# Kernel optimization log

Measured on AMD Instinct MI355X. Metric: run time of the kernel, lower is better.

Reference implementation:

```python
import jax, jax.numpy as jnp
import numpy as np

THRESH = 0.5  # original code thresholds raw span logit channel 0 at 0.5


def setup_inputs() -> dict:
    key = jax.random.key(0)
    ks = jax.random.split(key, 9)
    B, S, H, P = 4, 256, 768, 54  # P = num_spo_patterns + 1
    scale = 0.02
    return {
        "sequence_output": jax.random.normal(ks[0], (B, S, H), jnp.float32),
        "W1s": jax.random.normal(ks[1], (H, H), jnp.float32) * scale,
        "b1s": jnp.zeros((H,), jnp.float32),
        "W2s": jax.random.normal(ks[2], (2, H), jnp.float32) * scale,
        "b2s": jnp.zeros((2,), jnp.float32),
        "Wp1": jax.random.normal(ks[3], (H, 2 * H), jnp.float32) * scale,
        "bp1": jnp.zeros((H,), jnp.float32),
        "Wp2": jax.random.normal(ks[4], (P, H), jnp.float32) * scale,
        "bp2": jnp.zeros((P,), jnp.float32),
    }


def reference(sequence_output, W1s, b1s, W2s, b2s, Wp1, bp1, Wp2, bp2):
    x = sequence_output                                # [B,S,H]
    B, S, H = x.shape
    # span classifier: Linear -> ReLU -> Linear
    h = jax.nn.relu(jnp.einsum('bsh,kh->bsk', x, W1s) + b1s)
    span_logits = jnp.einsum('bsh,kh->bsk', h, W2s) + b2s   # [B,S,2]
    cand = span_logits[..., 0] > THRESH                      # [B,S] candidates
    # spo pattern classifier on concat pairs: Linear(2H,H) splits into two H->H maps
    Wa, Wb = Wp1[:, :H], Wp1[:, H:]                          # subject / object halves
    ha = jnp.einsum('bsh,kh->bsk', x, Wa)                    # [B,S,H]
    hb = jnp.einsum('bsh,kh->bsk', x, Wb)                    # [B,S,H]
    pair_hidden = jax.nn.relu(ha[:, :, None, :] + hb[:, None, :, :] + bp1)  # [B,S,S,H]
    pair_logits = jnp.einsum('bijh,ph->bijp', pair_hidden, Wp2) + bp2       # [B,S,S,P]
    # valid pairs: both are candidates and subj != obj (diagonal excluded)
    not_diag = ~jnp.eye(S, dtype=bool)
    valid = cand[:, :, None] & cand[:, None, :] & not_diag   # [B,S,S]
    # dense masked equivalent of the per-pair Python loop (invalid pairs zeroed,
    # matching the zeros fallback for empty candidate sets)
    spo_pattern_logits = jnp.where(valid[..., None], pair_logits, 0.0)
    return spo_pattern_logits
```

## Files before the change

kernel.cpp:

```cpp
#include <hip/hip_runtime.h>
#include <hip/hip_bf16.h>


#define M_ROWS 1024
#define HDIM 768
#define PDIM 54
#define MAXC 256
#define KSPLIT 4
#define KSEG (HDIM / KSPLIT)

#define CANDCNT_OFF  0
#define CANDIDX_OFF  1024
#define CANDSLOT_OFF 8192
#define HA_OFF       16384
#define HB_OFF       (16384 + 786432)
#define HPART_OFF    (16384 + 2 * 786432)

__global__ __launch_bounds__(256) void gemm_k_kernel(
    const float* __restrict__ x, const float* __restrict__ W1,
    float* __restrict__ hpart, int* __restrict__ candCnt)
{
    __shared__ float As[16][68];
    __shared__ float Bs[16][68];

    if (threadIdx.x == 0 && blockIdx.x == 0 && blockIdx.y == 0 && blockIdx.z == 0)
        *candCnt = 0;

    const int m0 = blockIdx.x * 64;
    const int n0 = blockIdx.y * 64;
    const int kb = blockIdx.z * KSEG;
    const int t  = threadIdx.x;
    const int tm = t & 15;
    const int tn = t >> 4;
    const int r  = t >> 2;
    const int c4 = (t & 3) * 4;

    float acc[4][4] = {};

    for (int k0 = kb; k0 < kb + KSEG; k0 += 16) {
        float4 av = *(const float4*)(x  + (size_t)(m0 + r) * HDIM + k0 + c4);
        float4 bv = *(const float4*)(W1 + (size_t)(n0 + r) * HDIM + k0 + c4);
        As[c4+0][r] = av.x; As[c4+1][r] = av.y; As[c4+2][r] = av.z; As[c4+3][r] = av.w;
        Bs[c4+0][r] = bv.x; Bs[c4+1][r] = bv.y; Bs[c4+2][r] = bv.z; Bs[c4+3][r] = bv.w;
        __syncthreads();
        #pragma unroll
        for (int kk = 0; kk < 16; ++kk) {
            float a[4], b[4];
            *(float4*)a = *(const float4*)&As[kk][tm * 4];
            *(float4*)b = *(const float4*)&Bs[kk][tn * 4];
            #pragma unroll
            for (int i = 0; i < 4; ++i)
                #pragma unroll
                for (int j = 0; j < 4; ++j)
                    acc[i][j] += a[i] * b[j];
        }
        __syncthreads();
    }

    float* dst = hpart + (size_t)blockIdx.z * (M_ROWS * HDIM);
    #pragma unroll
    for (int i = 0; i < 4; ++i) {
        float4 v = make_float4(acc[i][0], acc[i][1], acc[i][2], acc[i][3]);
        *(float4*)(dst + (size_t)(m0 + tm * 4 + i) * HDIM + n0 + tn * 4) = v;
    }
}

__global__ __launch_bounds__(256) void span_cand_kernel(
    const float* __restrict__ hpart, const float* __restrict__ b1,
    const float* __restrict__ w2row, const float* __restrict__ b2,
    int* __restrict__ candCount, int* __restrict__ candIdx,
    int* __restrict__ candSlot)
{
    const int m = blockIdx.x;
    const int t = threadIdx.x;
    float p = 0.f;
    for (int n = t; n < HDIM; n += 256) {
        float v = hpart[(size_t)m * HDIM + n]
                + hpart[(size_t)(M_ROWS * HDIM) + (size_t)m * HDIM + n]
                + hpart[(size_t)(2 * M_ROWS * HDIM) + (size_t)m * HDIM + n]
                + hpart[(size_t)(3 * M_ROWS * HDIM) + (size_t)m * HDIM + n];
        v += b1[n];
        v = v > 0.f ? v : 0.f;
        p += v * w2row[n];
    }
    __shared__ float wred[4];
    #pragma unroll
    for (int off = 32; off > 0; off >>= 1) p += __shfl_down(p, off, 64);
    if ((t & 63) == 0) wred[t >> 6] = p;
    __syncthreads();
    if (t == 0) {
        float s = wred[0] + wred[1] + wred[2] + wred[3] + b2[0];
        if (s > 0.5f) {
            int sl = atomicAdd(candCount, 1);
            if (sl < MAXC) { candIdx[sl] = m; candSlot[m] = sl; }
            else candSlot[m] = -1;
        } else {
            candSlot[m] = -1;
        }
    }
}

__global__ __launch_bounds__(256) void hab_kernel(
    const float* __restrict__ x, const float* __restrict__ Wp1,
    const int* __restrict__ candCount, const int* __restrict__ candIdx,
    float* __restrict__ ha, float* __restrict__ hb)
{
    int nc = *candCount; if (nc > MAXC) nc = MAXC;
    const int kk   = threadIdx.x >> 5;
    const int lane = threadIdx.x & 31;
    const int k    = blockIdx.x * 8 + kk;

    const float* wr = Wp1 + (size_t)k * (2 * HDIM);
    float4 wa[6], wb[6];
    #pragma unroll
    for (int c = 0; c < 6; ++c) {
        wa[c] = *(const float4*)(wr + c * 128 + lane * 4);
        wb[c] = *(const float4*)(wr + HDIM + c * 128 + lane * 4);
    }

    for (int slot = 0; slot < nc; ++slot) {
        int row = candIdx[slot];
        const float* xr = x + (size_t)row * HDIM;
        float sa = 0.f, sb = 0.f;
        #pragma unroll
        for (int c = 0; c < 6; ++c) {
            float4 xv = *(const float4*)(xr + c * 128 + lane * 4);
            sa += wa[c].x*xv.x + wa[c].y*xv.y + wa[c].z*xv.z + wa[c].w*xv.w;
            sb += wb[c].x*xv.x + wb[c].y*xv.y + wb[c].z*xv.z + wb[c].w*xv.w;
        }
        #pragma unroll
        for (int off = 16; off > 0; off >>= 1) {
            sa += __shfl_down(sa, off, 32);
            sb += __shfl_down(sb, off, 32);
        }
        if (lane == 0) {
            ha[(size_t)slot * HDIM + k] = sa;
            hb[(size_t)slot * HDIM + k] = sb;
        }
    }
}

__global__ __launch_bounds__(256) void pair_kernel(
    const float* __restrict__ ha, const float* __restrict__ hb,
    const float* __restrict__ bp1, const float* __restrict__ Wp2,
    const float* __restrict__ bp2, const int* __restrict__ candSlot,
    float* __restrict__ out)
{
    __shared__ int plist[512];
    __shared__ int pcnt;
    __shared__ float v[HDIM];
    __shared__ float red[4][PDIM + 2];
    const int t = threadIdx.x;

    float* outb = out + (size_t)blockIdx.x * 512 * PDIM;
    float4 z = make_float4(0.f, 0.f, 0.f, 0.f);
    #pragma unroll
    for (int q = 0; q < 27; ++q)
        *(float4*)(outb + (size_t)(q * 256 + t) * 4) = z;

    if (t == 0) pcnt = 0;
    __syncthreads();

    #pragma unroll
    for (int q = 0; q < 2; ++q) {
        int idx = blockIdx.x * 512 + q * 256 + t;
        int b = idx >> 16;
        int i = (idx >> 8) & 255;
        int j = idx & 255;
        if (i != j && candSlot[b * 256 + i] >= 0 && candSlot[b * 256 + j] >= 0) {
            int p = atomicAdd(&pcnt, 1);
            plist[p] = idx;
        }
    }
    __syncthreads();
    const int np = pcnt;

    for (int p = 0; p < np; ++p) {
        int idx = plist[p];
        int b = idx >> 16;
        int i = (idx >> 8) & 255;
        int j = idx & 255;
        int si = candSlot[b * 256 + i];
        int sj = candSlot[b * 256 + j];
        if (t < 192) {
            float4 a4 = *(const float4*)(ha + (size_t)si * HDIM + t * 4);
            float4 b4 = *(const float4*)(hb + (size_t)sj * HDIM + t * 4);
            float4 c4 = *(const float4*)(bp1 + t * 4);
            float4 r;
            r.x = a4.x + b4.x + c4.x; r.x = r.x > 0.f ? r.x : 0.f;
            r.y = a4.y + b4.y + c4.y; r.y = r.y > 0.f ? r.y : 0.f;
            r.z = a4.z + b4.z + c4.z; r.z = r.z > 0.f ? r.z : 0.f;
            r.w = a4.w + b4.w + c4.w; r.w = r.w > 0.f ? r.w : 0.f;
            *(float4*)(v + t * 4) = r;
        }
        __syncthreads();
        if (t < 216) {
            int pp  = t % PDIM;
            int seg = t / PDIM;
            const float* w  = Wp2 + (size_t)pp * HDIM + seg * 192;
            const float* vv = v + seg * 192;
            float s = 0.f;
            for (int h = 0; h < 192; h += 4) {
                float4 a  = *(const float4*)(vv + h);
                float4 b2 = *(const float4*)(w + h);
                s += a.x * b2.x + a.y * b2.y + a.z * b2.z + a.w * b2.w;
            }
            red[seg][pp] = s;
        }
        __syncthreads();
        if (t < PDIM)
            out[(size_t)idx * PDIM + t] = red[0][t] + red[1][t] + red[2][t] + red[3][t] + bp2[t];
        __syncthreads();
    }
}

extern "C" void kernel_launch(void* const* d_in, const int* in_sizes, int n_in,
                              void* d_out, int out_size, void* d_ws, size_t ws_size,
                              hipStream_t stream) {
    const float* x   = (const float*)d_in[0];
    const float* W1s = (const float*)d_in[1];
    const float* b1s = (const float*)d_in[2];
    const float* W2s = (const float*)d_in[3];
    const float* b2s = (const float*)d_in[4];
    const float* Wp1 = (const float*)d_in[5];
    const float* bp1 = (const float*)d_in[6];
    const float* Wp2 = (const float*)d_in[7];
    const float* bp2 = (const float*)d_in[8];

    char* ws = (char*)d_ws;
    int*   candCnt  = (int*)(ws + CANDCNT_OFF);
    int*   candIdx  = (int*)(ws + CANDIDX_OFF);
    int*   candSlot = (int*)(ws + CANDSLOT_OFF);
    float* ha       = (float*)(ws + HA_OFF);
    float* hb       = (float*)(ws + HB_OFF);
    float* hpart    = (float*)(ws + HPART_OFF);
    float* out = (float*)d_out;

    dim3 g(M_ROWS / 64, HDIM / 64, KSPLIT);
    gemm_k_kernel<<<g, 256, 0, stream>>>(x, W1s, hpart, candCnt);

    span_cand_kernel<<<M_ROWS, 256, 0, stream>>>(hpart, b1s, W2s, b2s,
                                                 candCnt, candIdx, candSlot);

    hab_kernel<<<96, 256, 0, stream>>>(x, Wp1, candCnt, candIdx, ha, hb);

    pair_kernel<<<512, 256, 0, stream>>>(ha, hb, bp1, Wp2, bp2, candSlot, out);
}
```

Baseline: 147.4 us.

## Fuse four stages into one cooperative persistent kernel with grid syncs

Replaces the four separate launches (split-K GEMM, span candidate scoring, ha/hb projection, pair classifier) with a single cooperative kernel of 768 blocks that uses grid.sync between phases. It also spreads the ha/hb projection over 8x more blocks by striding candidate slots, and halves the pair chunk size to 256 pairs per block. The goal is to remove launch gaps and the underutilised 96-block hab stage. In exchange it adds grid-wide barriers and requires all 768 blocks to be co-resident, falling back to the old launches if the cooperative launch fails.

```diff
diff --git a/kernel.cpp b/kernel.cpp
--- a/kernel.cpp
+++ b/kernel.cpp
@@ -1,5 +1,7 @@
 #include <hip/hip_runtime.h>
 #include <hip/hip_bf16.h>
+#include <hip/hip_cooperative_groups.h>
+namespace cg = cooperative_groups;
 
 
 #define M_ROWS 1024
@@ -8,6 +10,7 @@
 #define MAXC 256
 #define KSPLIT 4
 #define KSEG (HDIM / KSPLIT)
+#define GRID_C 768
 
 #define CANDCNT_OFF  0
 #define CANDIDX_OFF  1024
@@ -16,27 +19,213 @@
 #define HB_OFF       (16384 + 786432)
 #define HPART_OFF    (16384 + 2 * 786432)
 
+union SMem {
+    struct { float As[16][68]; float Bs[16][68]; } g;
+    struct { float wred[4]; } s;
+    struct { float v[HDIM]; float red[4][PDIM + 2]; int plist[256]; int pcnt; } p;
+};
+
+__global__ __launch_bounds__(256) void fused_kernel(
+    const float* __restrict__ x, const float* __restrict__ W1,
+    const float* __restrict__ b1, const float* __restrict__ w2row,
+    const float* __restrict__ b2, const float* __restrict__ Wp1,
+    const float* __restrict__ bp1, const float* __restrict__ Wp2,
+    const float* __restrict__ bp2,
+    float* __restrict__ hpart, int* __restrict__ candCnt,
+    int* __restrict__ candIdx, int* __restrict__ candSlot,
+    float* __restrict__ ha, float* __restrict__ hb,
+    float* __restrict__ out)
+{
+    __shared__ SMem sm;
+    cg::grid_group grid = cg::this_grid();
+    const int bid = blockIdx.x;
+    const int t   = threadIdx.x;
+
+    if (bid == 0 && t == 0) *candCnt = 0;
+    {
+        const int mt = bid & 15;
+        const int nt = (bid >> 4) % 12;
+        const int z  = bid / 192;
+        const int m0 = mt * 64, n0 = nt * 64, kb = z * KSEG;
+        const int tm = t & 15, tn = t >> 4;
+        const int r  = t >> 2, c4 = (t & 3) * 4;
+
+        float acc[4][4] = {};
+        for (int k0 = kb; k0 < kb + KSEG; k0 += 16) {
+            float4 av = *(const float4*)(x  + (size_t)(m0 + r) * HDIM + k0 + c4);
+            float4 bv = *(const float4*)(W1 + (size_t)(n0 + r) * HDIM + k0 + c4);
+            sm.g.As[c4+0][r] = av.x; sm.g.As[c4+1][r] = av.y; sm.g.As[c4+2][r] = av.z; sm.g.As[c4+3][r] = av.w;
+            sm.g.Bs[c4+0][r] = bv.x; sm.g.Bs[c4+1][r] = bv.y; sm.g.Bs[c4+2][r] = bv.z; sm.g.Bs[c4+3][r] = bv.w;
+            __syncthreads();
+            #pragma unroll
+            for (int kk = 0; kk < 16; ++kk) {
+                float a[4], b[4];
+                *(float4*)a = *(const float4*)&sm.g.As[kk][tm * 4];
+                *(float4*)b = *(const float4*)&sm.g.Bs[kk][tn * 4];
+                #pragma unroll
+                for (int i = 0; i < 4; ++i)
+                    #pragma unroll
+                    for (int j = 0; j < 4; ++j)
+                        acc[i][j] += a[i] * b[j];
+            }
+            __syncthreads();
+        }
+        float* dst = hpart + (size_t)z * (M_ROWS * HDIM);
+        #pragma unroll
+        for (int i = 0; i < 4; ++i) {
+            float4 v = make_float4(acc[i][0], acc[i][1], acc[i][2], acc[i][3]);
+            *(float4*)(dst + (size_t)(m0 + tm * 4 + i) * HDIM + n0 + tn * 4) = v;
+        }
+    }
+    grid.sync();
+
+    for (int m = bid; m < M_ROWS; m += GRID_C) {
+        float p = 0.f;
+        for (int n = t; n < HDIM; n += 256) {
+            float v = hpart[(size_t)m * HDIM + n]
+                    + hpart[(size_t)(M_ROWS * HDIM) + (size_t)m * HDIM + n]
+                    + hpart[(size_t)(2 * M_ROWS * HDIM) + (size_t)m * HDIM + n]
+                    + hpart[(size_t)(3 * M_ROWS * HDIM) + (size_t)m * HDIM + n];
+            v += b1[n];
+            v = v > 0.f ? v : 0.f;
+            p += v * w2row[n];
+        }
+        #pragma unroll
+        for (int off = 32; off > 0; off >>= 1) p += __shfl_down(p, off, 64);
+        if ((t & 63) == 0) sm.s.wred[t >> 6] = p;
+        __syncthreads();
+        if (t == 0) {
+            float s = sm.s.wred[0] + sm.s.wred[1] + sm.s.wred[2] + sm.s.wred[3] + b2[0];
+            if (s > 0.5f) {
+                int sl = atomicAdd(candCnt, 1);
+                if (sl < MAXC) { candIdx[sl] = m; candSlot[m] = sl; }
+                else candSlot[m] = -1;
+            } else {
+                candSlot[m] = -1;
+            }
+        }
+        __syncthreads();
+    }
+    grid.sync();
+
+    {
+        int nc = *candCnt; if (nc > MAXC) nc = MAXC;
+        const int kc   = bid % 96;
+        const int s0   = bid / 96;
+        const int kk   = t >> 5;
+        const int lane = t & 31;
+        const int k    = kc * 8 + kk;
+
+        const float* wr = Wp1 + (size_t)k * (2 * HDIM);
+        float4 wa[6], wb[6];
+        #pragma unroll
+        for (int c = 0; c < 6; ++c) {
+            wa[c] = *(const float4*)(wr + c * 128 + lane * 4);
+            wb[c] = *(const float4*)(wr + HDIM + c * 128 + lane * 4);
+        }
+        for (int slot = s0; slot < nc; slot += 8) {
+            int row = candIdx[slot];
+            const float* xr = x + (size_t)row * HDIM;
+            float sa = 0.f, sb = 0.f;
+            #pragma unroll
+            for (int c = 0; c < 6; ++c) {
+                float4 xv = *(const float4*)(xr + c * 128 + lane * 4);
+                sa += wa[c].x*xv.x + wa[c].y*xv.y + wa[c].z*xv.z + wa[c].w*xv.w;
+                sb += wb[c].x*xv.x + wb[c].y*xv.y + wb[c].z*xv.z + wb[c].w*xv.w;
+            }
+            #pragma unroll
+            for (int off = 16; off > 0; off >>= 1) {
+                sa += __shfl_down(sa, off, 32);
+                sb += __shfl_down(sb, off, 32);
+            }
+            if (lane == 0) {
+                ha[(size_t)slot * HDIM + k] = sa;
+                hb[(size_t)slot * HDIM + k] = sb;
+            }
+        }
+    }
+    grid.sync();
+
+    for (int chunk = bid; chunk < 1024; chunk += GRID_C) {
+        float* outb = out + (size_t)chunk * 256 * PDIM;
+        float4 z4 = make_float4(0.f, 0.f, 0.f, 0.f);
+        #pragma unroll
+        for (int q = 0; q < 14; ++q) {
+            int idx4 = q * 256 + t;
+            if (idx4 < 3456) *(float4*)(outb + (size_t)idx4 * 4) = z4;
+        }
+        if (t == 0) sm.p.pcnt = 0;
+        __syncthreads();
+
+        {
+            int idx = chunk * 256 + t;
+            int b = idx >> 16;
+            int i = (idx >> 8) & 255;
+            int j = idx & 255;
+            if (i != j && candSlot[b * 256 + i] >= 0 && candSlot[b * 256 + j] >= 0) {
+                int p = atomicAdd(&sm.p.pcnt, 1);
+                sm.p.plist[p] = idx;
+            }
+        }
+        __syncthreads();
+        const int np = sm.p.pcnt;
+
+        for (int p = 0; p < np; ++p) {
+            int idx = sm.p.plist[p];
+            int b = idx >> 16;
+            int i = (idx >> 8) & 255;
+            int j = idx & 255;
+            int si = candSlot[b * 256 + i];
+            int sj = candSlot[b * 256 + j];
+            if (t < 192) {
+                float4 a4 = *(const float4*)(ha + (size_t)si * HDIM + t * 4);
+                float4 b4 = *(const float4*)(hb + (size_t)sj * HDIM + t * 4);
+                float4 c4 = *(const float4*)(bp1 + t * 4);
+                float4 r;
+                r.x = a4.x + b4.x + c4.x; r.x = r.x > 0.f ? r.x : 0.f;
+                r.y = a4.y + b4.y + c4.y; r.y = r.y > 0.f ? r.y : 0.f;
+                r.z = a4.z + b4.z + c4.z; r.z = r.z > 0.f ? r.z : 0.f;
+                r.w = a4.w + b4.w + c4.w; r.w = r.w > 0.f ? r.w : 0.f;
+                *(float4*)(sm.p.v + t * 4) = r;
+            }
+            __syncthreads();
+            if (t < 216) {
+                int pp  = t % PDIM;
+                int seg = t / PDIM;
+                const float* w  = Wp2 + (size_t)pp * HDIM + seg * 192;
+                const float* vv = sm.p.v + seg * 192;
+                float s = 0.f;
+                for (int h = 0; h < 192; h += 4) {
+                    float4 a  = *(const float4*)(vv + h);
+                    float4 b2v = *(const float4*)(w + h);
+                    s += a.x * b2v.x + a.y * b2v.y + a.z * b2v.z + a.w * b2v.w;
+                }
+                sm.p.red[seg][pp] = s;
+            }
+            __syncthreads();
+            if (t < PDIM)
+                out[(size_t)idx * PDIM + t] = sm.p.red[0][t] + sm.p.red[1][t]
+                                            + sm.p.red[2][t] + sm.p.red[3][t] + bp2[t];
+            __syncthreads();
+        }
+    }
+}
+
 __global__ __launch_bounds__(256) void gemm_k_kernel(
     const float* __restrict__ x, const float* __restrict__ W1,
     float* __restrict__ hpart, int* __restrict__ candCnt)
 {
     __shared__ float As[16][68];
     __shared__ float Bs[16][68];
-
     if (threadIdx.x == 0 && blockIdx.x == 0 && blockIdx.y == 0 && blockIdx.z == 0)
         *candCnt = 0;
-
     const int m0 = blockIdx.x * 64;
     const int n0 = blockIdx.y * 64;
     const int kb = blockIdx.z * KSEG;
     const int t  = threadIdx.x;
-    const int tm = t & 15;
-    const int tn = t >> 4;
-    const int r  = t >> 2;
-    const int c4 = (t & 3) * 4;
-
+    const int tm = t & 15, tn = t >> 4;
+    const int r  = t >> 2, c4 = (t & 3) * 4;
     float acc[4][4] = {};
-
     for (int k0 = kb; k0 < kb + KSEG; k0 += 16) {
         float4 av = *(const float4*)(x  + (size_t)(m0 + r) * HDIM + k0 + c4);
         float4 bv = *(const float4*)(W1 + (size_t)(n0 + r) * HDIM + k0 + c4);
@@ -56,7 +245,6 @@
         }
         __syncthreads();
     }
-
     float* dst = hpart + (size_t)blockIdx.z * (M_ROWS * HDIM);
     #pragma unroll
     for (int i = 0; i < 4; ++i) {
@@ -109,7 +297,6 @@
     const int kk   = threadIdx.x >> 5;
     const int lane = threadIdx.x & 31;
     const int k    = blockIdx.x * 8 + kk;
-
     const float* wr = Wp1 + (size_t)k * (2 * HDIM);
     float4 wa[6], wb[6];
     #pragma unroll
@@ -117,7 +304,6 @@
         wa[c] = *(const float4*)(wr + c * 128 + lane * 4);
         wb[c] = *(const float4*)(wr + HDIM + c * 128 + lane * 4);
     }
-
     for (int slot = 0; slot < nc; ++slot) {
         int row = candIdx[slot];
         const float* xr = x + (size_t)row * HDIM;
@@ -151,16 +337,13 @@
     __shared__ float v[HDIM];
     __shared__ float red[4][PDIM + 2];
     const int t = threadIdx.x;
-
     float* outb = out + (size_t)blockIdx.x * 512 * PDIM;
     float4 z = make_float4(0.f, 0.f, 0.f, 0.f);
     #pragma unroll
     for (int q = 0; q < 27; ++q)
         *(float4*)(outb + (size_t)(q * 256 + t) * 4) = z;
-
     if (t == 0) pcnt = 0;
     __syncthreads();
-
     #pragma unroll
     for (int q = 0; q < 2; ++q) {
         int idx = blockIdx.x * 512 + q * 256 + t;
@@ -174,7 +357,6 @@
     }
     __syncthreads();
     const int np = pcnt;
-
     for (int p = 0; p < np; ++p) {
         int idx = plist[p];
         int b = idx >> 16;
@@ -236,13 +418,21 @@
     float* hpart    = (float*)(ws + HPART_OFF);
     float* out = (float*)d_out;
 
-    dim3 g(M_ROWS / 64, HDIM / 64, KSPLIT);
-    gemm_k_kernel<<<g, 256, 0, stream>>>(x, W1s, hpart, candCnt);
-
-    span_cand_kernel<<<M_ROWS, 256, 0, stream>>>(hpart, b1s, W2s, b2s,
-                                                 candCnt, candIdx, candSlot);
-
-    hab_kernel<<<96, 256, 0, stream>>>(x, Wp1, candCnt, candIdx, ha, hb);
-
-    pair_kernel<<<512, 256, 0, stream>>>(ha, hb, bp1, Wp2, bp2, candSlot, out);
-}
+    void* kargs[] = {
+        (void*)&x, (void*)&W1s, (void*)&b1s, (void*)&W2s, (void*)&b2s,
+        (void*)&Wp1, (void*)&bp1, (void*)&Wp2, (void*)&bp2,
+        (void*)&hpart, (void*)&candCnt, (void*)&candIdx, (void*)&candSlot,
+        (void*)&ha, (void*)&hb, (void*)&out
+    };
+    hipError_t err = hipLaunchCooperativeKernel((const void*)fused_kernel,
+                                                dim3(GRID_C), dim3(256),
+                                                kargs, 0, stream);
+    if (err != hipSuccess) {
+        dim3 g(M_ROWS / 64, HDIM / 64, KSPLIT);
+        gemm_k_kernel<<<g, 256, 0, stream>>>(x, W1s, hpart, candCnt);
+        span_cand_kernel<<<M_ROWS, 256, 0, stream>>>(hpart, b1s, W2s, b2s,
+                                                     candCnt, candIdx, candSlot);
+        hab_kernel<<<96, 256, 0, stream>>>(x, Wp1, candCnt, candIdx, ha, hb);
+        pair_kernel<<<512, 256, 0, stream>>>(ha, hb, bp1, Wp2, bp2, candSlot, out);
+    }
+}
```

Measured after the change: 436.6 us. 196% more time.
